# Kernel tuning notes

Measured on AMD Instinct MI355X. Metric: run time of the kernel, lower is better.

## Reference

```python
import jax, jax.numpy as jnp
import numpy as np
from jax import lax


def _conv(x, w, b, padding):
    # x: NCHW, w: OIHW
    y = lax.conv_general_dilated(x, w, (1, 1), padding,
                                 dimension_numbers=('NCHW', 'OIHW', 'NCHW'))
    return y + b[None, :, None, None]


def setup_inputs() -> dict:
    key = jax.random.key(0)
    ks = jax.random.split(key, 24)
    B = 64
    d = {
        'p2': jax.random.normal(ks[0], (B, 128, 64, 128), jnp.float32),
        'p3': jax.random.normal(ks[1], (B, 128, 32, 64), jnp.float32),
        'p4': jax.random.normal(ks[2], (B, 128, 16, 32), jnp.float32),
        'p5': jax.random.normal(ks[3], (B, 512, 8, 16), jnp.float32),
    }
    def w(k, shape, fan_in):
        return jax.random.normal(k, shape, jnp.float32) * (1.0 / np.sqrt(fan_in))
    # smooth convs 3x3, 128->128
    for i, name in enumerate(['s1', 's2', 's3']):
        d['w_' + name] = w(ks[4 + 2 * i], (128, 128, 3, 3), 128 * 9)
        d['b_' + name] = jnp.zeros((128,), jnp.float32)
    # tidy convs 1x1
    tidy_cin = [128, 128, 128, 512]
    for i in range(4):
        d['w_t%d' % (i + 1)] = w(ks[10 + i], (1, tidy_cin[i], 1, 1), tidy_cin[i])
        d['b_t%d' % (i + 1)] = jnp.zeros((1,), jnp.float32)
    # pl convs (kH,1) on single channel
    pl_kh = [64, 32, 16, 8]
    for i in range(4):
        d['w_pl%d' % (i + 1)] = w(ks[14 + i], (1, 1, pl_kh[i], 1), pl_kh[i])
        d['b_pl%d' % (i + 1)] = jnp.zeros((1,), jnp.float32)
    return d


def reference(p2, p3, p4, p5,
              w_s1, b_s1, w_s2, b_s2, w_s3, b_s3,
              w_t1, b_t1, w_t2, b_t2, w_t3, b_t3, w_t4, b_t4,
              w_pl1, b_pl1, w_pl2, b_pl2, w_pl3, b_pl3, w_pl4, b_pl4):
    B = p2.shape[0]
    # smooth + relu (p5 has no smooth in the original module)
    q2 = jax.nn.relu(_conv(p2, w_s1, b_s1, 'SAME'))
    q3 = jax.nn.relu(_conv(p3, w_s2, b_s2, 'SAME'))
    q4 = jax.nn.relu(_conv(p4, w_s3, b_s3, 'SAME'))
    # tidy 1x1 -> single score channel
    t1 = _conv(q2, w_t1, b_t1, 'VALID')
    t2 = _conv(q3, w_t2, b_t2, 'VALID')
    t3 = _conv(q4, w_t3, b_t3, 'VALID')
    t4 = _conv(p5, w_t4, b_t4, 'VALID')
    # column-pooling convs collapse height to 1 -> per-column scores
    c1 = _conv(t1, w_pl1, b_pl1, 'VALID').reshape(B, -1)  # [B,128]
    c2 = _conv(t2, w_pl2, b_pl2, 'VALID').reshape(B, -1)  # [B,64]
    c3 = _conv(t3, w_pl3, b_pl3, 'VALID').reshape(B, -1)  # [B,32]
    c4 = _conv(t4, w_pl4, b_pl4, 'VALID').reshape(B, -1)  # [B,16]
    return jnp.concatenate([c1, c2, c3, c4], axis=1)      # [B,240]
```

## Files before the change

kernel.cpp:

```cpp
#include <hip/hip_runtime.h>


typedef short s8v __attribute__((ext_vector_type(8)));
typedef float f4v __attribute__((ext_vector_type(4)));

#define BARRIER() asm volatile("s_waitcnt lgkmcnt(0)\n\ts_barrier" ::: "memory")

__device__ __forceinline__ unsigned short f32_bf16_rne(float f) {
  union { float f; unsigned int u; } v;
  v.f = f;
  unsigned int u = v.u;
  u += 0x7FFFu + ((u >> 16) & 1u);
  return (unsigned short)(u >> 16);
}

__global__ void prep_w_k(const float* __restrict__ w1,
                         const float* __restrict__ w2,
                         const float* __restrict__ w3,
                         unsigned short* __restrict__ out) {
  int idx = blockIdx.x * 256 + threadIdx.x;
  if (idx >= 442368) return;
  int i    = idx & 7;
  int cout = (idx >> 3) & 127;
  int t    = idx >> 10;
  int qg = t & 3; t >>= 2;
  int kw = t % 3; t /= 3;
  int kh = t % 3; t /= 3;
  int chunk = t & 3; t >>= 2;
  int s = t;
  const float* w = (s == 0) ? w1 : ((s == 1) ? w2 : w3);
  int cin = chunk * 32 + qg * 8 + i;
  out[idx] = f32_bf16_rne(w[((cout * 128 + cin) * 3 + kh) * 3 + kw]);
}

__global__ void init_out_k(float* __restrict__ out,
                           const float* bt1, const float* bt2,
                           const float* bt3, const float* bt4,
                           const float* wpl1, const float* bpl1,
                           const float* wpl2, const float* bpl2,
                           const float* wpl3, const float* bpl3,
                           const float* wpl4, const float* bpl4) {
  int idx = blockIdx.x * 256 + threadIdx.x;
  if (idx >= 64 * 240) return;
  int c = idx % 240;
  const float* wpl; const float* bpl; const float* bt; int H;
  if (c < 128)      { wpl = wpl1; bpl = bpl1; bt = bt1; H = 64; }
  else if (c < 192) { wpl = wpl2; bpl = bpl2; bt = bt2; H = 32; }
  else if (c < 224) { wpl = wpl3; bpl = bpl3; bt = bt3; H = 16; }
  else              { wpl = wpl4; bpl = bpl4; bt = bt4; H = 8;  }
  float s = 0.f;
  for (int h = 0; h < H; ++h) s += wpl[h];
  out[idx] = bt[0] * s + bpl[0];
}

__global__ void level4_k(const float* __restrict__ p5,
                         const float* __restrict__ w_t4,
                         const float* __restrict__ w_pl4,
                         float* __restrict__ out) {
  int b = blockIdx.x;
  int z = blockIdx.y;
  int t = threadIdx.x;
  int w = t & 15, g = t >> 4;
  const float* base = p5 + (size_t)b * 65536 + z * 16384;
  const float* wt = w_t4 + z * 128;
  float acc = 0.f;
  for (int j = g; j < 1024; j += 16) {
    acc += wt[j >> 3] * w_pl4[j & 7] * base[j * 16 + w];
  }
  acc += __shfl_xor(acc, 16);
  acc += __shfl_xor(acc, 32);
  if ((t & 48) == 0) atomicAdd(&out[b * 240 + 224 + w], acc);
}

template<int H, int W, int COLBASE>
__global__ __launch_bounds__(256, 2)
void conv_fused_k(const float* __restrict__ p,
                  const unsigned short* __restrict__ wl,
                  const float* __restrict__ b_s,
                  const float* __restrict__ w_t,
                  const float* __restrict__ w_pl,
                  float* __restrict__ out) {
  constexpr int WP = W + 2;
  constexpr int NT = (W >= 128) ? 2 : 1;
  constexpr int AW = W / (16 * NT);
  constexpr int HW = H * W;
  constexpr int SLOTS = 4 * W;
  constexpr int SPT = (SLOTS + 255) / 256;
  __shared__ __align__(16) unsigned short Xs[4][3][WP][8];
  __shared__ __align__(16) unsigned short Ws[2][3][4][128][8];

  const int tid = threadIdx.x;
  const int wave = tid >> 6, lane = tid & 63;
  const int lm = lane & 15, q = lane >> 4;
  const int h0 = blockIdx.x;
  const int b  = blockIdx.y;
  const float* pb = p + (size_t)b * 128 * HW;

  int sqg[SPT], swp[SPT];
  bool sok[SPT];
  const float* sbase[SPT];
#pragma unroll
  for (int k = 0; k < SPT; ++k) {
    int slot = tid + 256 * k;
    sok[k] = (SLOTS % 256 == 0) ? true : (slot < SLOTS);
    int qg = slot / W;
    int wp_ = slot % W;
    sqg[k] = qg; swp[k] = wp_;
    sbase[k] = pb + (size_t)(qg * 8) * HW + wp_;
  }
  bool rok[3]; int hin[3];
#pragma unroll
  for (int r = 0; r < 3; ++r) { hin[r] = h0 + r - 1; rok[r] = (hin[r] >= 0) && (hin[r] < H); }

  float xf[SPT][8];
  s8v wreg[6];
  const unsigned short* wseg = wl + wave * 512 + lane * 8;
  unsigned short* wdstbase = &Ws[0][0][0][0][0] + wave * 512 + lane * 8;

  auto issueW = [&](int t) {
    const unsigned short* s = wseg + t * 12288;
#pragma unroll
    for (int j = 0; j < 6; ++j) wreg[j] = *(const s8v*)(s + j * 2048);
  };
  auto writeW = [&](int buf) {
    unsigned short* d = wdstbase + buf * 12288;
#pragma unroll
    for (int j = 0; j < 6; ++j) *(s8v*)(d + j * 2048) = wreg[j];
  };
  auto issueXa = [&](float (*arr)[8], int c, int r) {
#pragma unroll
    for (int k = 0; k < SPT; ++k) {
      if (sok[k] && rok[r]) {
        const float* s = sbase[k] + (size_t)(c * 32) * HW + (size_t)hin[r] * W;
#pragma unroll
        for (int i = 0; i < 8; ++i) arr[k][i] = s[(size_t)i * HW];
      } else {
#pragma unroll
        for (int i = 0; i < 8; ++i) arr[k][i] = 0.f;
      }
    }
  };
  auto writeXa = [&](float (*arr)[8], int r) {
#pragma unroll
    for (int k = 0; k < SPT; ++k) {
      if (sok[k]) {
        s8v v;
#pragma unroll
        for (int i = 0; i < 8; ++i) v[i] = (short)f32_bf16_rne(arr[k][i]);
        *(s8v*)&Xs[sqg[k]][r][1 + swp[k]][0] = v;
      }
    }
  };

  if (tid < 24) {
    int qg = tid / 6, r2 = tid % 6;
    const s8v Z = {0, 0, 0, 0, 0, 0, 0, 0};
    *(s8v*)&Xs[qg][r2 >> 1][(r2 & 1) ? (WP - 1) : 0][0] = Z;
  }
  {
    float xr0[SPT][8], xr1[SPT][8];
    issueW(0);
    issueXa(xr0, 0, 0);
    issueXa(xr1, 0, 1);
    issueXa(xf, 0, 2);
    writeW(0);
    issueW(1);
    writeXa(xr0, 0);
    writeXa(xr1, 1);
  }
  BARRIER();

  f4v acc[8][NT];
#pragma unroll
  for (int mt = 0; mt < 8; ++mt)
#pragma unroll
    for (int t = 0; t < NT; ++t)
      acc[mt][t] = (f4v){0.f, 0.f, 0.f, 0.f};

  for (int c = 0; c < 4; ++c) {
#pragma unroll
    for (int kh = 0; kh < 3; ++kh) {
      const int sidx = c * 3 + kh;
      if (!(c == 3 && kh == 2)) writeW((sidx + 1) & 1);
      if (!(c == 3 && kh >= 1)) issueW(sidx + 2);
      if (kh == 0) {
        writeXa(xf, 2);
        if (c < 3) issueXa(xf, c + 1, 0);
      } else if (kh == 1) {
        if (c < 3) { writeXa(xf, 0); issueXa(xf, c + 1, 1); }
      } else {
        if (c < 3) { writeXa(xf, 1); issueXa(xf, c + 1, 2); }
      }
      if (wave < AW) {
        const unsigned short* WsRd = &Ws[sidx & 1][0][0][0][0];
#pragma unroll
        for (int kw = 0; kw < 3; ++kw) {
          s8v bfv[NT];
#pragma unroll
          for (int t = 0; t < NT; ++t) {
            int n = wave * (16 * NT) + t * 16 + lm;
            bfv[t] = *(const s8v*)&Xs[q][kh][n + kw][0];
          }
#pragma unroll
          for (int mt = 0; mt < 8; ++mt) {
            s8v af = *(const s8v*)(WsRd + kw * 4096 + q * 1024 + (mt * 16 + lm) * 8);
#pragma unroll
            for (int t = 0; t < NT; ++t)
              acc[mt][t] = __builtin_amdgcn_mfma_f32_16x16x32_bf16(af, bfv[t], acc[mt][t], 0, 0, 0);
          }
        }
      }
      if (!(c == 3 && kh == 2)) BARRIER();
    }
  }

  if (wave < AW) {
    const float wph = w_pl[h0];
#pragma unroll
    for (int t = 0; t < NT; ++t) {
      float s = 0.f;
#pragma unroll
      for (int mt = 0; mt < 8; ++mt) {
#pragma unroll
        for (int rg = 0; rg < 4; ++rg) {
          int cout = mt * 16 + q * 4 + rg;
          float v = fmaxf(acc[mt][t][rg] + b_s[cout], 0.f);
          s = fmaf(w_t[cout], v, s);
        }
      }
      s *= wph;
      s += __shfl_xor(s, 16);
      s += __shfl_xor(s, 32);
      int n = wave * (16 * NT) + t * 16 + lm;
      if (lane < 16) atomicAdd(&out[b * 240 + COLBASE + n], s);
    }
  }
}

extern "C" void kernel_launch(void* const* d_in, const int* in_sizes, int n_in,
                              void* d_out, int out_size, void* d_ws, size_t ws_size,
                              hipStream_t stream) {
  (void)in_sizes; (void)n_in; (void)out_size; (void)ws_size;
  const float* p2   = (const float*)d_in[0];
  const float* p3   = (const float*)d_in[1];
  const float* p4   = (const float*)d_in[2];
  const float* p5   = (const float*)d_in[3];
  const float* w_s1 = (const float*)d_in[4];
  const float* b_s1 = (const float*)d_in[5];
  const float* w_s2 = (const float*)d_in[6];
  const float* b_s2 = (const float*)d_in[7];
  const float* w_s3 = (const float*)d_in[8];
  const float* b_s3 = (const float*)d_in[9];
  const float* w_t1 = (const float*)d_in[10];
  const float* b_t1 = (const float*)d_in[11];
  const float* w_t2 = (const float*)d_in[12];
  const float* b_t2 = (const float*)d_in[13];
  const float* w_t3 = (const float*)d_in[14];
  const float* b_t3 = (const float*)d_in[15];
  const float* w_t4 = (const float*)d_in[16];
  const float* b_t4 = (const float*)d_in[17];
  const float* w_pl1 = (const float*)d_in[18];
  const float* b_pl1 = (const float*)d_in[19];
  const float* w_pl2 = (const float*)d_in[20];
  const float* b_pl2 = (const float*)d_in[21];
  const float* w_pl3 = (const float*)d_in[22];
  const float* b_pl3 = (const float*)d_in[23];
  const float* w_pl4 = (const float*)d_in[24];
  const float* b_pl4 = (const float*)d_in[25];

  unsigned short* wp = (unsigned short*)d_ws;
  float* out = (float*)d_out;

  prep_w_k<<<dim3(1728), dim3(256), 0, stream>>>(w_s1, w_s2, w_s3, wp);
  init_out_k<<<dim3(60), dim3(256), 0, stream>>>(out, b_t1, b_t2, b_t3, b_t4,
                                                 w_pl1, b_pl1, w_pl2, b_pl2,
                                                 w_pl3, b_pl3, w_pl4, b_pl4);
  conv_fused_k<64, 128, 0><<<dim3(64, 64), dim3(256), 0, stream>>>(
      p2, wp, b_s1, w_t1, w_pl1, out);
  conv_fused_k<32, 64, 128><<<dim3(32, 64), dim3(256), 0, stream>>>(
      p3, wp + 147456, b_s2, w_t2, w_pl2, out);
  conv_fused_k<16, 32, 192><<<dim3(16, 64), dim3(256), 0, stream>>>(
      p4, wp + 294912, b_s3, w_t3, w_pl3, out);
  level4_k<<<dim3(64, 4), dim3(256), 0, stream>>>(p5, w_t4, w_pl4, out);
}
```

Measured before the change: 647.3 us.

## Compute four output rows per block with 512 threads and shared row halo

Each conv block now produces four output rows instead of one and loads a six-row input halo into double-buffered shared memory. This cuts redundant input reloads (each row was previously loaded three times) and amortises the weight staging across more MFMA work. Waves are split over both the output-channel tiles and the column tiles. The block grows to 512 threads, the per-row pooling weights are folded in before a single atomic per column, and s_setprio is raised around the MFMA loop. The trade-off is more LDS and register pressure per block and fewer blocks in the grid.

```diff
diff --git a/kernel.cpp b/kernel.cpp
--- a/kernel.cpp
+++ b/kernel.cpp
@@ -73,65 +73,71 @@
 }
 
 template<int H, int W, int COLBASE>
-__global__ __launch_bounds__(256, 2)
+__global__ __launch_bounds__(512, 2)
 void conv_fused_k(const float* __restrict__ p,
                   const unsigned short* __restrict__ wl,
                   const float* __restrict__ b_s,
                   const float* __restrict__ w_t,
                   const float* __restrict__ w_pl,
                   float* __restrict__ out) {
+  constexpr int R  = 4;
   constexpr int WP = W + 2;
-  constexpr int NT = (W >= 128) ? 2 : 1;
-  constexpr int AW = W / (16 * NT);
   constexpr int HW = H * W;
-  constexpr int SLOTS = 4 * W;
-  constexpr int SPT = (SLOTS + 255) / 256;
-  __shared__ __align__(16) unsigned short Xs[4][3][WP][8];
+  constexpr int WN = W / 16;
+  constexpr int WM = 8 / WN;
+  constexpr int MT = 8 / WM;
+  constexpr int SLOTS = 2 * 4 * W;
+  constexpr int SPT = (SLOTS + 511) / 512;
+
+  __shared__ __align__(16) unsigned short Xs[2][4][6][WP][8];
   __shared__ __align__(16) unsigned short Ws[2][3][4][128][8];
 
-  const int tid = threadIdx.x;
+  const int tid  = threadIdx.x;
   const int wave = tid >> 6, lane = tid & 63;
   const int lm = lane & 15, q = lane >> 4;
-  const int h0 = blockIdx.x;
+  const int mw = wave / WN, ns = wave % WN;
+  const int hb = blockIdx.x * R;
   const int b  = blockIdx.y;
   const float* pb = p + (size_t)b * 128 * HW;
 
-  int sqg[SPT], swp[SPT];
   bool sok[SPT];
+  int  h0k[SPT];
+  int  xbase[SPT];
   const float* sbase[SPT];
 #pragma unroll
   for (int k = 0; k < SPT; ++k) {
-    int slot = tid + 256 * k;
-    sok[k] = (SLOTS % 256 == 0) ? true : (slot < SLOTS);
-    int qg = slot / W;
-    int wp_ = slot % W;
-    sqg[k] = qg; swp[k] = wp_;
-    sbase[k] = pb + (size_t)(qg * 8) * HW + wp_;
-  }
-  bool rok[3]; int hin[3];
-#pragma unroll
-  for (int r = 0; r < 3; ++r) { hin[r] = h0 + r - 1; rok[r] = (hin[r] >= 0) && (hin[r] < H); }
+    int slot = tid + 512 * k;
+    sok[k] = (SLOTS % 512 == 0) ? true : (slot < SLOTS);
+    int rk = slot / (4 * W);
+    int qg = (slot / W) & 3;
+    int wp = slot % W;
+    h0k[k]   = hb - 1 + rk;
+    xbase[k] = ((qg * 6 + rk) * WP + 1 + wp) * 8;
+    sbase[k] = pb + (size_t)(qg * 8) * HW + wp;
+  }
 
   float xf[SPT][8];
-  s8v wreg[6];
-  const unsigned short* wseg = wl + wave * 512 + lane * 8;
-  unsigned short* wdstbase = &Ws[0][0][0][0][0] + wave * 512 + lane * 8;
+  s8v wreg[3];
+  const unsigned short* wseg = wl + tid * 24;
+  unsigned short* wdst = &Ws[0][0][0][0][0] + tid * 24;
 
   auto issueW = [&](int t) {
     const unsigned short* s = wseg + t * 12288;
 #pragma unroll
-    for (int j = 0; j < 6; ++j) wreg[j] = *(const s8v*)(s + j * 2048);
+    for (int j = 0; j < 3; ++j) wreg[j] = *(const s8v*)(s + j * 8);
   };
   auto writeW = [&](int buf) {
-    unsigned short* d = wdstbase + buf * 12288;
-#pragma unroll
-    for (int j = 0; j < 6; ++j) *(s8v*)(d + j * 2048) = wreg[j];
-  };
-  auto issueXa = [&](float (*arr)[8], int c, int r) {
+    unsigned short* d = wdst + buf * 12288;
+#pragma unroll
+    for (int j = 0; j < 3; ++j) *(s8v*)(d + j * 8) = wreg[j];
+  };
+  auto issueXa = [&](float (*arr)[8], int chunk, int kh) {
 #pragma unroll
     for (int k = 0; k < SPT; ++k) {
-      if (sok[k] && rok[r]) {
-        const float* s = sbase[k] + (size_t)(c * 32) * HW + (size_t)hin[r] * W;
+      int hin = h0k[k] + 2 * kh;
+      bool ok = sok[k] && ((unsigned)hin < (unsigned)H);
+      if (ok) {
+        const float* s = sbase[k] + (size_t)chunk * (32 * HW) + (size_t)hin * W;
 #pragma unroll
         for (int i = 0; i < 8; ++i) arr[k][i] = s[(size_t)i * HW];
       } else {
@@ -140,101 +146,102 @@
       }
     }
   };
-  auto writeXa = [&](float (*arr)[8], int r) {
+  auto writeXa = [&](float (*arr)[8], int buf, int kh) {
+    unsigned short* dst = &Xs[buf][0][0][0][0] + 2 * kh * (WP * 8);
 #pragma unroll
     for (int k = 0; k < SPT; ++k) {
       if (sok[k]) {
         s8v v;
 #pragma unroll
         for (int i = 0; i < 8; ++i) v[i] = (short)f32_bf16_rne(arr[k][i]);
-        *(s8v*)&Xs[sqg[k]][r][1 + swp[k]][0] = v;
-      }
-    }
-  };
-
-  if (tid < 24) {
-    int qg = tid / 6, r2 = tid % 6;
+        *(s8v*)(dst + xbase[k]) = v;
+      }
+    }
+  };
+
+  if (tid < 96) {
+    int t = tid;
+    int pos = (t & 1) ? (WP - 1) : 0; t >>= 1;
+    int sl = t % 6; t /= 6;
+    int qg = t & 3; int bf = t >> 2;
     const s8v Z = {0, 0, 0, 0, 0, 0, 0, 0};
-    *(s8v*)&Xs[qg][r2 >> 1][(r2 & 1) ? (WP - 1) : 0][0] = Z;
+    *(s8v*)&Xs[bf][qg][sl][pos][0] = Z;
   }
   {
-    float xr0[SPT][8], xr1[SPT][8];
+    float x0[SPT][8], x1[SPT][8], x2[SPT][8];
     issueW(0);
-    issueXa(xr0, 0, 0);
-    issueXa(xr1, 0, 1);
-    issueXa(xf, 0, 2);
+    issueXa(x0, 0, 0);
+    issueXa(x1, 0, 1);
+    issueXa(x2, 0, 2);
     writeW(0);
     issueW(1);
-    writeXa(xr0, 0);
-    writeXa(xr1, 1);
+    writeXa(x0, 0, 0);
+    writeXa(x1, 0, 1);
+    writeXa(x2, 0, 2);
+    issueXa(xf, 1, 0);
   }
   BARRIER();
 
-  f4v acc[8][NT];
-#pragma unroll
-  for (int mt = 0; mt < 8; ++mt)
-#pragma unroll
-    for (int t = 0; t < NT; ++t)
-      acc[mt][t] = (f4v){0.f, 0.f, 0.f, 0.f};
+  f4v acc[R][MT];
+#pragma unroll
+  for (int r = 0; r < R; ++r)
+#pragma unroll
+    for (int mt = 0; mt < MT; ++mt)
+      acc[r][mt] = (f4v){0.f, 0.f, 0.f, 0.f};
+
+  const int ncol = ns * 16 + lm;
 
   for (int c = 0; c < 4; ++c) {
 #pragma unroll
     for (int kh = 0; kh < 3; ++kh) {
       const int sidx = c * 3 + kh;
-      if (!(c == 3 && kh == 2)) writeW((sidx + 1) & 1);
-      if (!(c == 3 && kh >= 1)) issueW(sidx + 2);
-      if (kh == 0) {
-        writeXa(xf, 2);
-        if (c < 3) issueXa(xf, c + 1, 0);
-      } else if (kh == 1) {
-        if (c < 3) { writeXa(xf, 0); issueXa(xf, c + 1, 1); }
-      } else {
-        if (c < 3) { writeXa(xf, 1); issueXa(xf, c + 1, 2); }
-      }
-      if (wave < AW) {
-        const unsigned short* WsRd = &Ws[sidx & 1][0][0][0][0];
-#pragma unroll
-        for (int kw = 0; kw < 3; ++kw) {
-          s8v bfv[NT];
-#pragma unroll
-          for (int t = 0; t < NT; ++t) {
-            int n = wave * (16 * NT) + t * 16 + lm;
-            bfv[t] = *(const s8v*)&Xs[q][kh][n + kw][0];
-          }
-#pragma unroll
-          for (int mt = 0; mt < 8; ++mt) {
-            s8v af = *(const s8v*)(WsRd + kw * 4096 + q * 1024 + (mt * 16 + lm) * 8);
-#pragma unroll
-            for (int t = 0; t < NT; ++t)
-              acc[mt][t] = __builtin_amdgcn_mfma_f32_16x16x32_bf16(af, bfv[t], acc[mt][t], 0, 0, 0);
-          }
+      if (sidx < 11) writeW((sidx + 1) & 1);
+      if (sidx < 10) issueW(sidx + 2);
+      if (c < 3) writeXa(xf, (c + 1) & 1, kh);
+      if (kh < 2) { if (c < 3) issueXa(xf, c + 1, kh + 1); }
+      else        { if (c < 2) issueXa(xf, c + 2, 0); }
+
+      const unsigned short* WsRd = &Ws[sidx & 1][0][0][0][0];
+      const unsigned short* XsRd = &Xs[c & 1][0][0][0][0];
+      __builtin_amdgcn_s_setprio(1);
+#pragma unroll
+      for (int kw = 0; kw < 3; ++kw) {
+        s8v af[MT];
+#pragma unroll
+        for (int mt = 0; mt < MT; ++mt)
+          af[mt] = *(const s8v*)(WsRd + kw * 4096 + q * 1024 +
+                                 ((mw * MT + mt) * 16 + lm) * 8);
+#pragma unroll
+        for (int r = 0; r < R; ++r) {
+          const s8v bfv = *(const s8v*)(XsRd + ((q * 6 + (kh + r)) * WP + (ncol + kw)) * 8);
+#pragma unroll
+          for (int mt = 0; mt < MT; ++mt)
+            acc[r][mt] = __builtin_amdgcn_mfma_f32_16x16x32_bf16(af[mt], bfv, acc[r][mt], 0, 0, 0);
         }
       }
-      if (!(c == 3 && kh == 2)) BARRIER();
-    }
-  }
-
-  if (wave < AW) {
-    const float wph = w_pl[h0];
-#pragma unroll
-    for (int t = 0; t < NT; ++t) {
-      float s = 0.f;
-#pragma unroll
-      for (int mt = 0; mt < 8; ++mt) {
-#pragma unroll
-        for (int rg = 0; rg < 4; ++rg) {
-          int cout = mt * 16 + q * 4 + rg;
-          float v = fmaxf(acc[mt][t][rg] + b_s[cout], 0.f);
-          s = fmaf(w_t[cout], v, s);
-        }
-      }
-      s *= wph;
-      s += __shfl_xor(s, 16);
-      s += __shfl_xor(s, 32);
-      int n = wave * (16 * NT) + t * 16 + lm;
-      if (lane < 16) atomicAdd(&out[b * 240 + COLBASE + n], s);
-    }
-  }
+      __builtin_amdgcn_s_setprio(0);
+      if (sidx < 11) BARRIER();
+    }
+  }
+
+  float stot = 0.f;
+#pragma unroll
+  for (int r = 0; r < R; ++r) {
+    float s = 0.f;
+#pragma unroll
+    for (int mt = 0; mt < MT; ++mt) {
+#pragma unroll
+      for (int rg = 0; rg < 4; ++rg) {
+        int cout = (mw * MT + mt) * 16 + q * 4 + rg;
+        float v = fmaxf(acc[r][mt][rg] + b_s[cout], 0.f);
+        s = fmaf(w_t[cout], v, s);
+      }
+    }
+    stot = fmaf(w_pl[hb + r], s, stot);
+  }
+  stot += __shfl_xor(stot, 16);
+  stot += __shfl_xor(stot, 32);
+  if (lane < 16) atomicAdd(&out[b * 240 + COLBASE + ncol], stot);
 }
 
 extern "C" void kernel_launch(void* const* d_in, const int* in_sizes, int n_in,
@@ -275,11 +282,11 @@
   init_out_k<<<dim3(60), dim3(256), 0, stream>>>(out, b_t1, b_t2, b_t3, b_t4,
                                                  w_pl1, b_pl1, w_pl2, b_pl2,
                                                  w_pl3, b_pl3, w_pl4, b_pl4);
-  conv_fused_k<64, 128, 0><<<dim3(64, 64), dim3(256), 0, stream>>>(
+  conv_fused_k<64, 128, 0><<<dim3(16, 64), dim3(512), 0, stream>>>(
       p2, wp, b_s1, w_t1, w_pl1, out);
-  conv_fused_k<32, 64, 128><<<dim3(32, 64), dim3(256), 0, stream>>>(
+  conv_fused_k<32, 64, 128><<<dim3(8, 64), dim3(512), 0, stream>>>(
       p3, wp + 147456, b_s2, w_t2, w_pl2, out);
-  conv_fused_k<16, 32, 192><<<dim3(16, 64), dim3(256), 0, stream>>>(
+  conv_fused_k<16, 32, 192><<<dim3(4, 64), dim3(512), 0, stream>>>(
       p4, wp + 294912, b_s3, w_t3, w_pl3, out);
   level4_k<<<dim3(64, 4), dim3(256), 0, stream>>>(p5, w_t4, w_pl4, out);
 }
```

Measured after the change: 734.6 us. 1.13x slower.
